# Optimization experiments

Hardware: AMD Instinct MI355X
Metric: run time of the kernel (lower is better)

## Reference

```python
import jax, jax.numpy as jnp
import numpy as np

N = 8192


def setup_inputs() -> dict:
    key = jax.random.key(0)
    k1, k2 = jax.random.split(key)
    pos = jax.random.uniform(k1, (N, 2), dtype=jnp.float32)          # nn.init.uniform_ on [N,2] param
    dist = jax.random.uniform(k2, (N, N), dtype=jnp.float32)         # target graph distances [N,N]
    return {"pos": pos, "dist": dist}


def reference(pos, dist):
    # pairwise differences: [N, N, 2]  (broadcasted1 - broadcasted2 in torch code)
    diff = pos[None, :, :] - pos[:, None, :]
    sq = jnp.sum(diff * diff, axis=-1)                               # [N, N]
    # safe sqrt: torch.norm has subgradient 0 at 0 (diagonal); guard to stay grad-safe
    pred_dist = jnp.where(sq > 0, jnp.sqrt(jnp.where(sq > 0, sq, 1.0)), 0.0)
    mask = dist != 0
    pred_dist = jnp.where(mask, pred_dist, dist)
    safe_dist = jnp.where(mask, dist, 1.0)                           # avoid 0-division; masked anyway
    stress_matrix = jnp.where(mask, jnp.square((pred_dist - dist) / safe_dist), dist)
    return jnp.sum(stress_matrix)
```

## Files before the change

kernel.cpp:

```cpp
#include <hip/hip_runtime.h>

#define NDIM 8192
#define ROWS_PER_BLOCK 4
#define BLOCK 256
#define GRID (NDIM / ROWS_PER_BLOCK)
#define COLS_PER_THREAD 8

__global__ __launch_bounds__(BLOCK) void stress_partial_kernel(
    const float* __restrict__ pos,
    const float* __restrict__ dist,
    float* __restrict__ partials)
{
    const int row0 = blockIdx.x * ROWS_PER_BLOCK;

    float pix[ROWS_PER_BLOCK], piy[ROWS_PER_BLOCK];
#pragma unroll
    for (int r = 0; r < ROWS_PER_BLOCK; ++r) {
        pix[r] = pos[2 * (row0 + r)];
        piy[r] = pos[2 * (row0 + r) + 1];
    }

    float acc = 0.0f;

    for (int jb = threadIdx.x * COLS_PER_THREAD; jb < NDIM; jb += BLOCK * COLS_PER_THREAD) {
        float pjx[COLS_PER_THREAD], pjy[COLS_PER_THREAD];
#pragma unroll
        for (int q = 0; q < 4; ++q) {
            const float4 p = *(const float4*)(pos + 2 * jb + 4 * q);
            pjx[2 * q]     = p.x;  pjy[2 * q]     = p.y;
            pjx[2 * q + 1] = p.z;  pjy[2 * q + 1] = p.w;
        }

#pragma unroll
        for (int r = 0; r < ROWS_PER_BLOCK; ++r) {
            const float* drow = dist + (size_t)(row0 + r) * NDIM + jb;
            const float4 d0 = *(const float4*)(drow);
            const float4 d1 = *(const float4*)(drow + 4);
            const float dv[COLS_PER_THREAD] = {d0.x, d0.y, d0.z, d0.w,
                                               d1.x, d1.y, d1.z, d1.w};
#pragma unroll
            for (int k = 0; k < COLS_PER_THREAD; ++k) {
                const float dx = pjx[k] - pix[r];
                const float dy = pjy[k] - piy[r];
                const float sq = dx * dx + dy * dy;
                const float pred = sqrtf(sq);
                const float d = dv[k];
                const float rcp = __builtin_amdgcn_rcpf(d);
                const float t = pred * rcp - 1.0f;
                acc += (d != 0.0f) ? t * t : 0.0f;
            }
        }
    }

#pragma unroll
    for (int off = 32; off > 0; off >>= 1)
        acc += __shfl_down(acc, off, 64);

    __shared__ float wave_sums[BLOCK / 64];
    const int lane = threadIdx.x & 63;
    const int wave = threadIdx.x >> 6;
    if (lane == 0) wave_sums[wave] = acc;
    __syncthreads();

    if (threadIdx.x == 0) {
        float s = 0.0f;
#pragma unroll
        for (int w = 0; w < BLOCK / 64; ++w) s += wave_sums[w];
        partials[blockIdx.x] = s;
    }
}

__global__ __launch_bounds__(BLOCK) void reduce_final_kernel(
    const float* __restrict__ partials,
    float* __restrict__ out)
{
    float acc = 0.0f;
#pragma unroll
    for (int i = 0; i < GRID / BLOCK; ++i)
        acc += partials[threadIdx.x + i * BLOCK];

#pragma unroll
    for (int off = 32; off > 0; off >>= 1)
        acc += __shfl_down(acc, off, 64);

    __shared__ float wave_sums[BLOCK / 64];
    const int lane = threadIdx.x & 63;
    const int wave = threadIdx.x >> 6;
    if (lane == 0) wave_sums[wave] = acc;
    __syncthreads();

    if (threadIdx.x == 0) {
        float s = 0.0f;
#pragma unroll
        for (int w = 0; w < BLOCK / 64; ++w) s += wave_sums[w];
        out[0] = s;
    }
}

extern "C" void kernel_launch(void* const* d_in, const int* in_sizes, int n_in,
                              void* d_out, int out_size, void* d_ws, size_t ws_size,
                              hipStream_t stream)
{
    const float* pos  = (const float*)d_in[0];
    const float* dist = (const float*)d_in[1];
    float* out = (float*)d_out;
    float* partials = (float*)d_ws;

    stress_partial_kernel<<<GRID, BLOCK, 0, stream>>>(pos, dist, partials);
    reduce_final_kernel<<<1, BLOCK, 0, stream>>>(partials, out);
}
```

Before: 353.8 us.

## Software-pipeline dist loads with double buffering and nontemporal loads

Unrolls the column loop into four fixed iterations with double-buffered register sets, so the loads for the next tile are issued before the current tile is computed. The dist loads become nontemporal because the data is streamed once. The arithmetic switches to raw hardware sqrt and fused multiply-adds, with one accumulator per row to break the dependency chain. Register pressure rises with the doubled buffers, and the fixed iteration count hardcodes NDIM/TILE_STRIDE = 4.

```diff
diff --git a/kernel.cpp b/kernel.cpp
--- a/kernel.cpp
+++ b/kernel.cpp
@@ -4,7 +4,11 @@
 #define ROWS_PER_BLOCK 4
 #define BLOCK 256
 #define GRID (NDIM / ROWS_PER_BLOCK)
-#define COLS_PER_THREAD 8
+#define CPT 8
+#define TILE_STRIDE (BLOCK * CPT)
+#define NITER (NDIM / TILE_STRIDE)
+
+typedef float fx4 __attribute__((ext_vector_type(4)));
 
 __global__ __launch_bounds__(BLOCK) void stress_partial_kernel(
     const float* __restrict__ pos,
@@ -12,6 +16,7 @@
     float* __restrict__ partials)
 {
     const int row0 = blockIdx.x * ROWS_PER_BLOCK;
+    const int jb0  = threadIdx.x * CPT;
 
     float pix[ROWS_PER_BLOCK], piy[ROWS_PER_BLOCK];
 #pragma unroll
@@ -20,37 +25,64 @@
         piy[r] = pos[2 * (row0 + r) + 1];
     }
 
-    float acc = 0.0f;
+    float accr[ROWS_PER_BLOCK] = {0.0f, 0.0f, 0.0f, 0.0f};
 
-    for (int jb = threadIdx.x * COLS_PER_THREAD; jb < NDIM; jb += BLOCK * COLS_PER_THREAD) {
-        float pjx[COLS_PER_THREAD], pjy[COLS_PER_THREAD];
+    fx4 dA[ROWS_PER_BLOCK][2], dB[ROWS_PER_BLOCK][2];
+    fx4 pA[4], pB[4];
+
+    auto LOAD = [&](int it, fx4 (&dreg)[ROWS_PER_BLOCK][2], fx4 (&preg)[4]) {
+        const int jb = jb0 + it * TILE_STRIDE;
+#pragma unroll
+        for (int q = 0; q < 4; ++q)
+            preg[q] = *(const fx4*)(pos + 2 * jb + 4 * q);
+#pragma unroll
+        for (int r = 0; r < ROWS_PER_BLOCK; ++r) {
+            const fx4* drow =
+                (const fx4*)(dist + (size_t)(row0 + r) * NDIM + jb);
+            dreg[r][0] = __builtin_nontemporal_load(drow);
+            dreg[r][1] = __builtin_nontemporal_load(drow + 1);
+        }
+    };
+
+    auto COMPUTE = [&](const fx4 (&dreg)[ROWS_PER_BLOCK][2],
+                       const fx4 (&preg)[4]) {
+        float pjx[CPT], pjy[CPT];
 #pragma unroll
         for (int q = 0; q < 4; ++q) {
-            const float4 p = *(const float4*)(pos + 2 * jb + 4 * q);
-            pjx[2 * q]     = p.x;  pjy[2 * q]     = p.y;
-            pjx[2 * q + 1] = p.z;  pjy[2 * q + 1] = p.w;
+            pjx[2 * q]     = preg[q].x;  pjy[2 * q]     = preg[q].y;
+            pjx[2 * q + 1] = preg[q].z;  pjy[2 * q + 1] = preg[q].w;
         }
-
 #pragma unroll
         for (int r = 0; r < ROWS_PER_BLOCK; ++r) {
-            const float* drow = dist + (size_t)(row0 + r) * NDIM + jb;
-            const float4 d0 = *(const float4*)(drow);
-            const float4 d1 = *(const float4*)(drow + 4);
-            const float dv[COLS_PER_THREAD] = {d0.x, d0.y, d0.z, d0.w,
-                                               d1.x, d1.y, d1.z, d1.w};
+            const float dv[CPT] = {dreg[r][0].x, dreg[r][0].y,
+                                   dreg[r][0].z, dreg[r][0].w,
+                                   dreg[r][1].x, dreg[r][1].y,
+                                   dreg[r][1].z, dreg[r][1].w};
 #pragma unroll
-            for (int k = 0; k < COLS_PER_THREAD; ++k) {
+            for (int k = 0; k < CPT; ++k) {
                 const float dx = pjx[k] - pix[r];
                 const float dy = pjy[k] - piy[r];
-                const float sq = dx * dx + dy * dy;
-                const float pred = sqrtf(sq);
+                const float sq = __builtin_fmaf(dx, dx, dy * dy);
+                const float pred = __builtin_amdgcn_sqrtf(sq);
                 const float d = dv[k];
-                const float rcp = __builtin_amdgcn_rcpf(d);
-                const float t = pred * rcp - 1.0f;
-                acc += (d != 0.0f) ? t * t : 0.0f;
+                const float t =
+                    __builtin_fmaf(pred, __builtin_amdgcn_rcpf(d), -1.0f);
+                const float z = (d != 0.0f) ? t : 0.0f;
+                accr[r] = __builtin_fmaf(z, z, accr[r]);
             }
         }
-    }
+    };
+
+    LOAD(0, dA, pA);
+    LOAD(1, dB, pB);
+    COMPUTE(dA, pA);
+    LOAD(2, dA, pA);
+    COMPUTE(dB, pB);
+    LOAD(3, dB, pB);
+    COMPUTE(dA, pA);
+    COMPUTE(dB, pB);
+
+    float acc = (accr[0] + accr[1]) + (accr[2] + accr[3]);
 
 #pragma unroll
     for (int off = 32; off > 0; off >>= 1)
```

After: 348.7 us. About the same (-1.5%).
